# Performance work log

Measured on AMD Instinct MI355X. Metric: run time of the kernel, lower is better.

## Reference

```python
import jax, jax.numpy as jnp
import numpy as np

TOPK, NUM_CLASSES, ALPHA, BETA, EPS = 13, 80, 1.0, 6.0, 1e-9
IOU_EPS = 1e-7  # eps used inside bbox_iou (ultralytics default)


def ciou(box1, box2):
    # box1, box2: broadcastable [..., 4] in xyxy format; returns CIoU [..., 1]
    b1x1, b1y1, b1x2, b1y2 = jnp.split(box1, 4, axis=-1)
    b2x1, b2y1, b2x2, b2y2 = jnp.split(box2, 4, axis=-1)
    w1, h1 = b1x2 - b1x1, b1y2 - b1y1 + IOU_EPS
    w2, h2 = b2x2 - b2x1, b2y2 - b2y1 + IOU_EPS
    inter = (jnp.clip(jnp.minimum(b1x2, b2x2) - jnp.maximum(b1x1, b2x1), 0.0) *
             jnp.clip(jnp.minimum(b1y2, b2y2) - jnp.maximum(b1y1, b2y1), 0.0))
    union = w1 * h1 + w2 * h2 - inter + IOU_EPS
    iou = inter / union
    cw = jnp.maximum(b1x2, b2x2) - jnp.minimum(b1x1, b2x1)  # enclosing box width
    ch = jnp.maximum(b1y2, b2y2) - jnp.minimum(b1y1, b2y1)
    c2 = cw ** 2 + ch ** 2 + IOU_EPS
    rho2 = ((b2x1 + b2x2 - b1x1 - b1x2) ** 2 + (b2y1 + b2y2 - b1y1 - b1y2) ** 2) / 4.0
    v = (4.0 / np.pi ** 2) * (jnp.arctan(w2 / h2) - jnp.arctan(w1 / h1)) ** 2
    alpha = jax.lax.stop_gradient(v / (v - iou + (1.0 + IOU_EPS)))  # torch: with no_grad
    return iou - (rho2 / c2 + v * alpha)


def tal_forward(pd_scores, pd_bboxes, anc_points, gt_labels, gt_bboxes, mask_gt):
    bs, na, nc = pd_scores.shape
    nb = gt_bboxes.shape[1]
    dt = pd_scores.dtype
    mgt = mask_gt[..., 0]  # (b, nb)

    # --- select_candidates_in_gts: anchor center strictly inside gt box ---
    lt, rb = gt_bboxes[..., :2], gt_bboxes[..., 2:]
    deltas = jnp.concatenate([anc_points[None, None, :, :] - lt[:, :, None, :],
                              rb[:, :, None, :] - anc_points[None, None, :, :]], axis=-1)  # (b,nb,na,4)
    mask_in_gts = (deltas.min(-1) > EPS).astype(dt)  # (b,nb,na)
    valid = (mask_in_gts * mgt[:, :, None]) > 0  # bool (b,nb,na)

    # --- get_box_metrics: class score gather + pairwise CIoU, masked ---
    lbl = gt_labels[..., 0].astype(jnp.int32)  # (b,nb)
    scores = jnp.take_along_axis(pd_scores, lbl[:, None, :], axis=2)  # (b,na,nb)
    bbox_scores = jnp.where(valid, scores.transpose(0, 2, 1), 0.0)  # (b,nb,na)
    ov = ciou(gt_bboxes[:, :, None, :], pd_bboxes[:, None, :, :])[..., 0]  # (b,nb,na)
    overlaps = jnp.where(valid, jnp.clip(ov, 0.0), 0.0)
    align_metric = bbox_scores ** ALPHA * overlaps ** BETA

    # --- select_topk_candidates ---
    _, tk_i = jax.lax.top_k(align_metric, TOPK)  # (b,nb,TOPK)
    tk_i = jnp.where(mgt[:, :, None] > 0, tk_i, 0)  # invalid gt rows -> all idx 0 (counted >1 -> zeroed)
    flat_i = tk_i.reshape(bs * nb, TOPK)
    cnt = jnp.zeros((bs * nb, na), jnp.int32).at[jnp.arange(bs * nb)[:, None], flat_i].add(1)
    cnt = cnt.reshape(bs, nb, na)
    is_in_topk = jnp.where(cnt > 1, 0, cnt).astype(dt)
    mask_pos = is_in_topk * mask_in_gts * mgt[:, :, None]

    # --- select_highest_overlaps: resolve anchors claimed by multiple gts ---
    fg = mask_pos.sum(-2)  # (b,na)
    mask_multi = fg[:, None, :] > 1
    max_idx = overlaps.argmax(1)  # (b,na)
    is_max = jax.nn.one_hot(max_idx, nb, dtype=dt).transpose(0, 2, 1)  # (b,nb,na)
    mask_pos = jnp.where(mask_multi, is_max, mask_pos)
    fg_mask = mask_pos.sum(-2)  # (b,na)
    target_gt_idx = mask_pos.argmax(-2)  # (b,na)

    # --- get_targets ---
    flat_gt_idx = target_gt_idx + jnp.arange(bs)[:, None] * nb  # (b,na)
    target_labels = jnp.clip(lbl.reshape(-1)[flat_gt_idx], 0)
    target_bboxes = gt_bboxes.reshape(-1, 4)[flat_gt_idx]  # (b,na,4)
    target_scores = jax.nn.one_hot(target_labels, nc, dtype=dt)
    target_scores = jnp.where(fg_mask[..., None] > 0, target_scores, 0.0)

    # --- normalization of align metric ---
    align_metric = align_metric * mask_pos
    pos_align = align_metric.max(-1, keepdims=True)  # (b,nb,1)
    pos_over = (overlaps * mask_pos).max(-1, keepdims=True)
    norm = (align_metric * pos_over / (pos_align + EPS)).max(-2)[..., None]  # (b,na,1)
    target_scores = target_scores * norm
    return target_labels, target_bboxes, target_scores, fg_mask > 0, target_gt_idx


def _make_boxes(key, shape):
    kc, kw = jax.random.split(key)
    c = jax.random.uniform(kc, shape[:-1] + (2,), jnp.float32, 60.0, 580.0)
    wh = jax.random.uniform(kw, shape[:-1] + (2,), jnp.float32, 20.0, 120.0)
    return jnp.concatenate([c - wh / 2, c + wh / 2], axis=-1)


def setup_inputs() -> dict:
    key = jax.random.key(0)
    ks = jax.random.split(key, 6)
    bs, na, nc, nb = 32, 8400, 80, 64
    pd_scores = jax.random.uniform(ks[0], (bs, na, nc), jnp.float32)
    pd_bboxes = _make_boxes(ks[1], (bs, na, 4))
    anc_points = jax.random.uniform(ks[2], (na, 2), jnp.float32, 0.0, 640.0)
    gt_labels = jax.random.randint(ks[3], (bs, nb, 1), 0, nc, dtype=jnp.int32)
    gt_bboxes = _make_boxes(ks[4], (bs, nb, 4))
    mask_gt = (jax.random.uniform(ks[5], (bs, nb, 1)) < 0.8).astype(jnp.float32)
    return {"pd_scores": pd_scores, "pd_bboxes": pd_bboxes, "anc_points": anc_points,
            "gt_labels": gt_labels, "gt_bboxes": gt_bboxes, "mask_gt": mask_gt}


def reference(pd_scores, pd_bboxes, anc_points, gt_labels, gt_bboxes, mask_gt):
    return tal_forward(pd_scores, pd_bboxes, anc_points, gt_labels, gt_bboxes, mask_gt)
```

## Files before the change

### kernel.cpp

```cpp
#include <hip/hip_runtime.h>
#include <stdint.h>

#pragma clang fp contract(off)

#define BS 32
#define NB 64
#define NA 8400
#define NC 80
#define TK 13
#define QCAP 640
#define CMAX (QCAP + 32)
#define FORCED 32

typedef float floatx4 __attribute__((ext_vector_type(4)));

__device__ __forceinline__ float ciou_f(float g0, float g1, float g2, float g3,
                                        float p0, float p1, float p2, float p3) {
    const float E = 1e-7f;
    float w1 = g2 - g0, h1 = (g3 - g1) + E;
    float w2 = p2 - p0, h2 = (p3 - p1) + E;
    float iw = fminf(g2, p2) - fmaxf(g0, p0); iw = fmaxf(iw, 0.f);
    float ih = fminf(g3, p3) - fmaxf(g1, p1); ih = fmaxf(ih, 0.f);
    float inter = iw * ih;
    float uni = w1 * h1 + w2 * h2 - inter + E;
    float iou = inter / uni;
    float cw = fmaxf(g2, p2) - fminf(g0, p0);
    float ch = fmaxf(g3, p3) - fminf(g1, p1);
    float c2 = cw * cw + ch * ch + E;
    float dx = p0 + p2 - g0 - g2;
    float dy = p1 + p3 - g1 - g3;
    float rho2 = (dx * dx + dy * dy) / 4.0f;
    float da = atanf(w2 / h2) - atanf(w1 / h1);
    float v = 0.4052847345693511f * (da * da);
    float alpha = v / ((v - iou) + 1.0000001f);
    return iou - (rho2 / c2 + v * alpha);
}

__global__ __launch_bounds__(256) void k1a_scan(
    const float* __restrict__ anc,
    const float* __restrict__ gt_bboxes,
    const float* __restrict__ mask_gt,
    int* __restrict__ qcnt, int* __restrict__ qlist)
{
    int b = blockIdx.y;
    int a = blockIdx.x * 256 + threadIdx.x;
    if (a >= NA) return;
    float2 ap = *(const float2*)&anc[2 * a];
    for (int j = 0; j < NB; j++) {
        int r = b * NB + j;
        float mg = mask_gt[r];
        float gx = gt_bboxes[r * 4 + 0], gy = gt_bboxes[r * 4 + 1];
        float gz = gt_bboxes[r * 4 + 2], gw = gt_bboxes[r * 4 + 3];
        float d0 = ap.x - gx, d1 = ap.y - gy, d2 = gz - ap.x, d3 = gw - ap.y;
        float dmin = fminf(fminf(d0, d1), fminf(d2, d3));
        if (mg > 0.f && dmin > 1e-9f) {
            int p = atomicAdd(&qcnt[r], 1);
            if (p < QCAP) qlist[r * QCAP + p] = a;
        }
    }
}

__global__ __launch_bounds__(64) void k1b_topk(
    const float* __restrict__ pd_scores,
    const float* __restrict__ pd_bboxes,
    const float* __restrict__ anc,
    const int* __restrict__ gt_labels,
    const float* __restrict__ gt_bboxes,
    const float* __restrict__ mask_gt,
    const int* __restrict__ qcnt, const int* __restrict__ qlist,
    int* __restrict__ tk_a, float* __restrict__ tk_v,
    float* __restrict__ tk_o, int* __restrict__ tk_f)
{
    int r = blockIdx.x;
    int b = r >> 6;
    int lane = threadIdx.x;

    if (mask_gt[r] <= 0.f) {
        if (lane < TK) {
            tk_a[r * TK + lane] = 0; tk_v[r * TK + lane] = 0.f;
            tk_o[r * TK + lane] = 0.f; tk_f[r * TK + lane] = 0;
        }
        return;
    }

    __shared__ int   ca[CMAX];
    __shared__ float cv[CMAX];
    __shared__ float co[CMAX];

    float4 g = *(const float4*)&gt_bboxes[r * 4];
    int lbl = gt_labels[r];
    int n0 = min(qcnt[r], QCAP);

    bool add = false;
    if (lane < FORCED) {
        float2 ap = *(const float2*)&anc[2 * lane];
        float d0 = ap.x - g.x, d1 = ap.y - g.y, d2 = g.z - ap.x, d3 = g.w - ap.y;
        float dmin = fminf(fminf(d0, d1), fminf(d2, d3));
        add = !(dmin > 1e-9f);
    }
    unsigned long long mb = __ballot(add);
    int pos = __popcll(mb & ((1ull << lane) - 1ull));
    if (add) { ca[n0 + pos] = lane; cv[n0 + pos] = 0.f; co[n0 + pos] = 0.f; }
    int n = n0 + __popcll(mb);

    for (int c = lane; c < n0; c += 64) {
        int a = qlist[r * QCAP + c];
        float4 p = *(const float4*)&pd_bboxes[(b * NA + a) * 4];
        float ov = fmaxf(ciou_f(g.x, g.y, g.z, g.w, p.x, p.y, p.z, p.w), 0.f);
        float sc = pd_scores[(b * NA + a) * NC + lbl];
        float o2 = ov * ov;
        ca[c] = a | (1 << 30); cv[c] = sc * (o2 * o2 * o2); co[c] = ov;
    }
    __syncthreads();

    unsigned consumed = 0;
    int wslot = 0; float wval = 0.f;
    for (int round = 0; round < TK; round++) {
        float bv = -2.f; int bgi = 0x7fffffff; int bsl = 0;
        int li = 0;
        for (int c = lane; c < n; c += 64, li++) {
            if (consumed & (1u << li)) continue;
            float v = cv[c]; int gi = ca[c] & 0x3fffffff;
            if (v > bv || (v == bv && gi < bgi)) { bv = v; bgi = gi; bsl = c; }
        }
        for (int off = 32; off; off >>= 1) {
            float v2 = __shfl_down(bv, off);
            int  gi2 = __shfl_down(bgi, off);
            int  sl2 = __shfl_down(bsl, off);
            if (v2 > bv || (v2 == bv && gi2 < bgi)) { bv = v2; bgi = gi2; bsl = sl2; }
        }
        int wsl = __shfl(bsl, 0);
        float wv = __shfl(bv, 0);
        if ((wsl & 63) == lane) consumed |= 1u << (wsl >> 6);
        if (lane == round) { wslot = wsl; wval = wv; }
    }
    if (lane < TK) {
        int packed = ca[wslot]; int a = packed & 0x3fffffff; int in = (packed >> 30) & 1;
        tk_a[r * TK + lane] = a;
        tk_v[r * TK + lane] = wval;
        tk_o[r * TK + lane] = co[wslot];
        tk_f[r * TK + lane] = in;
    }
}

__global__ void k2a_init(int* cnt, int* jA, unsigned* posA, unsigned* posO,
                         int* mcount, int* qcnt) {
    int i = blockIdx.x * 256 + threadIdx.x;
    if (i < BS * NA) { cnt[i] = 0; jA[i] = -1; }
    if (i < BS * NB) { posA[i] = 0u; posO[i] = 0u; qcnt[i] = 0; }
    if (i == 0) *mcount = 0;
}

__global__ void k2b_count(const int* __restrict__ tk_a, const int* __restrict__ tk_f,
                          int* __restrict__ cnt) {
    int c = blockIdx.x * 256 + threadIdx.x;
    if (c >= BS * NB * TK) return;
    if (!tk_f[c]) return;
    int r = c / TK; int b = r >> 6;
    atomicAdd(&cnt[b * NA + tk_a[c]], 1);
}

__global__ void k2c_single(const int* __restrict__ tk_a, const float* __restrict__ tk_v,
                           const float* __restrict__ tk_o, const int* __restrict__ tk_f,
                           const int* __restrict__ cnt, int* __restrict__ jA,
                           float* __restrict__ av,
                           unsigned* __restrict__ posA, unsigned* __restrict__ posO,
                           int* __restrict__ mlist, int* __restrict__ mcount) {
    int c = blockIdx.x * 256 + threadIdx.x;
    if (c >= BS * NB * TK) return;
    if (!tk_f[c]) return;
    int r = c / TK; int b = r >> 6; int j = r & 63;
    int a = tk_a[c];
    int i = b * NA + a;
    if (cnt[i] == 1) {
        jA[i] = j; av[i] = tk_v[c];
        atomicMax(&posA[b * NB + j], __float_as_uint(tk_v[c]));
        atomicMax(&posO[b * NB + j], __float_as_uint(tk_o[c]));
    } else {
        int old = atomicCAS(&jA[i], -1, -2);
        if (old == -1) { int p = atomicAdd(mcount, 1); mlist[p] = i; }
    }
}

__global__ __launch_bounds__(256) void k2d_multi(
    const float* __restrict__ pd_scores,
    const float* __restrict__ pd_bboxes,
    const float* __restrict__ anc,
    const int* __restrict__ gt_labels,
    const float* __restrict__ gt_bboxes,
    const float* __restrict__ mask_gt,
    const int* __restrict__ mlist, const int* __restrict__ mcount,
    int* __restrict__ jA, float* __restrict__ av,
    unsigned* __restrict__ posA, unsigned* __restrict__ posO)
{
    int wid = (blockIdx.x * 256 + threadIdx.x) >> 6;
    int lane = threadIdx.x & 63;
    int nwaves = (gridDim.x * 256) >> 6;
    int nm = *mcount;
    for (int e = wid; e < nm; e += nwaves) {
        int i = mlist[e];
        int b = i / NA, a = i - b * NA;
        float2 ap = *(const float2*)&anc[2 * a];
        int row = b * NB + lane;
        float o = 0.f;
        if (mask_gt[row] > 0.f) {
            float4 g = *(const float4*)&gt_bboxes[row * 4];
            float d0 = ap.x - g.x, d1 = ap.y - g.y, d2 = g.z - ap.x, d3 = g.w - ap.y;
            float dmin = fminf(fminf(d0, d1), fminf(d2, d3));
            if (dmin > 1e-9f) {
                float4 p = *(const float4*)&pd_bboxes[(b * NA + a) * 4];
                o = fmaxf(ciou_f(g.x, g.y, g.z, g.w, p.x, p.y, p.z, p.w), 0.f);
            }
        }
        float bv = o; int bj = lane;
        for (int off = 32; off; off >>= 1) {
            float v2 = __shfl_down(bv, off);
            int  j2 = __shfl_down(bj, off);
            if (v2 > bv || (v2 == bv && j2 < bj)) { bv = v2; bj = j2; }
        }
        if (lane == 0) {
            int lbl = gt_labels[b * NB + bj];
            float sc = pd_scores[(b * NA + a) * NC + lbl];
            float o2 = bv * bv;
            float alg = sc * (o2 * o2 * o2);
            jA[i] = bj; av[i] = alg;
            atomicMax(&posA[b * NB + bj], __float_as_uint(alg));
            atomicMax(&posO[b * NB + bj], __float_as_uint(bv));
        }
    }
}

__global__ void k2f_final(const int* __restrict__ gt_labels,
                          const float* __restrict__ gt_bboxes,
                          const int* __restrict__ jA, const float* __restrict__ av,
                          const unsigned* __restrict__ posA, const unsigned* __restrict__ posO,
                          float* __restrict__ out,
                          float* __restrict__ normw, int* __restrict__ clsw) {
    int i = blockIdx.x * 256 + threadIdx.x;
    if (i >= BS * NA) return;
    int b = i / NA;
    int jj = jA[i];
    int tg = jj < 0 ? 0 : jj;
    int lab = gt_labels[b * NB + tg]; lab = lab < 0 ? 0 : lab;

    float* o_lab  = out;
    float* o_bbox = out + BS * NA;
    float* o_fg   = out + BS * NA * (5 + NC);
    float* o_idx  = o_fg + BS * NA;

    o_lab[i] = (float)lab;
    float4 bb = *(const float4*)&gt_bboxes[(b * NB + tg) * 4];
    *(float4*)&o_bbox[i * 4] = bb;
    o_fg[i] = (jj >= 0) ? 1.f : 0.f;
    o_idx[i] = (float)tg;

    float nrm = 0.f;
    if (jj >= 0) {
        float pa = __uint_as_float(posA[b * NB + jj]);
        float po = __uint_as_float(posO[b * NB + jj]);
        nrm = (av[i] * po) / (pa + 1e-9f);
    }
    normw[i] = nrm;
    clsw[i] = (jj >= 0) ? lab : -1;
}

__global__ void k3_scores(const float* __restrict__ normw, const int* __restrict__ clsw,
                          float* __restrict__ out) {
    int t = blockIdx.x * 256 + threadIdx.x;
    int row = t / 20;
    int c4 = (t - row * 20) * 4;
    int cls = clsw[row];
    float nv = normw[row];
    floatx4 v;
    v.x = (c4 + 0 == cls) ? nv : 0.f;
    v.y = (c4 + 1 == cls) ? nv : 0.f;
    v.z = (c4 + 2 == cls) ? nv : 0.f;
    v.w = (c4 + 3 == cls) ? nv : 0.f;
    float* o_sc = out + BS * NA * 5;
    __builtin_nontemporal_store(v, (floatx4*)&o_sc[row * NC + c4]);
}

extern "C" void kernel_launch(void* const* d_in, const int* in_sizes, int n_in,
                              void* d_out, int out_size, void* d_ws, size_t ws_size,
                              hipStream_t stream) {
    const float* pd_scores = (const float*)d_in[0];
    const float* pd_bboxes = (const float*)d_in[1];
    const float* anc       = (const float*)d_in[2];
    const int*   gt_labels = (const int*)d_in[3];
    const float* gt_bboxes = (const float*)d_in[4];
    const float* mask_gt   = (const float*)d_in[5];
    float* out = (float*)d_out;

    char* w = (char*)d_ws;
    const int NCAND = BS * NB * TK;
    int*      tk_a = (int*)w;      w += NCAND * 4;
    int*      tk_f = (int*)w;      w += NCAND * 4;
    float*    tk_v = (float*)w;    w += NCAND * 4;
    float*    tk_o = (float*)w;    w += NCAND * 4;
    int*      cnt  = (int*)w;      w += BS * NA * 4;
    int*      jA   = (int*)w;      w += BS * NA * 4;
    float*    av   = (float*)w;    w += BS * NA * 4;
    unsigned* posA = (unsigned*)w; w += BS * NB * 4;
    unsigned* posO = (unsigned*)w; w += BS * NB * 4;
    float*    normw = (float*)w;   w += BS * NA * 4;
    int*      clsw  = (int*)w;     w += BS * NA * 4;
    int*      mlist = (int*)w;     w += NCAND * 4;
    int*      mcount = (int*)w;    w += 64;
    int*      qcnt  = (int*)w;     w += BS * NB * 4;
    int*      qlist = (int*)w;     w += BS * NB * QCAP * 4;

    k2a_init<<<(BS * NA + 255) / 256, 256, 0, stream>>>(cnt, jA, posA, posO,
                                                        mcount, qcnt);
    {
        dim3 g((NA + 255) / 256, BS);
        k1a_scan<<<g, 256, 0, stream>>>(anc, gt_bboxes, mask_gt, qcnt, qlist);
    }
    k1b_topk<<<BS * NB, 64, 0, stream>>>(pd_scores, pd_bboxes, anc, gt_labels,
                                         gt_bboxes, mask_gt, qcnt, qlist,
                                         tk_a, tk_v, tk_o, tk_f);
    k2b_count<<<(NCAND + 255) / 256, 256, 0, stream>>>(tk_a, tk_f, cnt);
    k2c_single<<<(NCAND + 255) / 256, 256, 0, stream>>>(tk_a, tk_v, tk_o, tk_f,
                                                        cnt, jA, av, posA, posO,
                                                        mlist, mcount);
    k2d_multi<<<52, 256, 0, stream>>>(pd_scores, pd_bboxes, anc, gt_labels,
                                      gt_bboxes, mask_gt, mlist, mcount,
                                      jA, av, posA, posO);
    k2f_final<<<(BS * NA + 255) / 256, 256, 0, stream>>>(gt_labels, gt_bboxes, jA, av,
                                                         posA, posO, out, normw, clsw);
    k3_scores<<<(BS * NA * NC / 4 + 255) / 256, 256, 0, stream>>>(normw, clsw, out);
}
```

Baseline: 253.0 us.

## Aggregate scan atomics per wave, fuse count and final kernels, memset init

The candidate scan now uses a wave ballot so that one atomicAdd per wave reserves queue slots, instead of one atomic per hit. The per-anchor count atomics move into the top-k kernel, and the per-anchor finalisation is folded into the score-writing kernel, removing the normw/clsw intermediates. The init kernel becomes a single hipMemsetAsync over a contiguous zeroed region, with jA re-encoded so that 0 means unassigned. This removes three launches and extra global traffic, but the fused final kernel recomputes per-row values in each of 20 threads and the queue slot order may differ.

```diff
diff --git a/kernel.cpp b/kernel.cpp
--- a/kernel.cpp
+++ b/kernel.cpp
@@ -44,18 +44,25 @@
 {
     int b = blockIdx.y;
     int a = blockIdx.x * 256 + threadIdx.x;
-    if (a >= NA) return;
-    float2 ap = *(const float2*)&anc[2 * a];
+    int lane = threadIdx.x & 63;
+    bool inrange = a < NA;
+    float2 ap = inrange ? *(const float2*)&anc[2 * a] : make_float2(-1.f, -1.f);
     for (int j = 0; j < NB; j++) {
         int r = b * NB + j;
         float mg = mask_gt[r];
-        float gx = gt_bboxes[r * 4 + 0], gy = gt_bboxes[r * 4 + 1];
-        float gz = gt_bboxes[r * 4 + 2], gw = gt_bboxes[r * 4 + 3];
-        float d0 = ap.x - gx, d1 = ap.y - gy, d2 = gz - ap.x, d3 = gw - ap.y;
+        float4 g = *(const float4*)&gt_bboxes[r * 4];
+        float d0 = ap.x - g.x, d1 = ap.y - g.y, d2 = g.z - ap.x, d3 = g.w - ap.y;
         float dmin = fminf(fminf(d0, d1), fminf(d2, d3));
-        if (mg > 0.f && dmin > 1e-9f) {
-            int p = atomicAdd(&qcnt[r], 1);
-            if (p < QCAP) qlist[r * QCAP + p] = a;
+        bool hit = inrange && (mg > 0.f) && (dmin > 1e-9f);
+        unsigned long long m = __ballot(hit);
+        if (m) {
+            int rank = __popcll(m & ((1ull << lane) - 1ull));
+            int ldr = __ffsll((long long)m) - 1;
+            int base = 0;
+            if (lane == ldr) base = atomicAdd(&qcnt[r], __popcll(m));
+            base = __shfl(base, ldr);
+            int p = base + rank;
+            if (hit && p < QCAP) qlist[r * QCAP + p] = a;
         }
     }
 }
@@ -69,7 +76,8 @@
     const float* __restrict__ mask_gt,
     const int* __restrict__ qcnt, const int* __restrict__ qlist,
     int* __restrict__ tk_a, float* __restrict__ tk_v,
-    float* __restrict__ tk_o, int* __restrict__ tk_f)
+    float* __restrict__ tk_o, int* __restrict__ tk_f,
+    int* __restrict__ cnt)
 {
     int r = blockIdx.x;
     int b = r >> 6;
@@ -140,24 +148,8 @@
         tk_v[r * TK + lane] = wval;
         tk_o[r * TK + lane] = co[wslot];
         tk_f[r * TK + lane] = in;
-    }
-}
-
-__global__ void k2a_init(int* cnt, int* jA, unsigned* posA, unsigned* posO,
-                         int* mcount, int* qcnt) {
-    int i = blockIdx.x * 256 + threadIdx.x;
-    if (i < BS * NA) { cnt[i] = 0; jA[i] = -1; }
-    if (i < BS * NB) { posA[i] = 0u; posO[i] = 0u; qcnt[i] = 0; }
-    if (i == 0) *mcount = 0;
-}
-
-__global__ void k2b_count(const int* __restrict__ tk_a, const int* __restrict__ tk_f,
-                          int* __restrict__ cnt) {
-    int c = blockIdx.x * 256 + threadIdx.x;
-    if (c >= BS * NB * TK) return;
-    if (!tk_f[c]) return;
-    int r = c / TK; int b = r >> 6;
-    atomicAdd(&cnt[b * NA + tk_a[c]], 1);
+        if (in) atomicAdd(&cnt[b * NA + a], 1);
+    }
 }
 
 __global__ void k2c_single(const int* __restrict__ tk_a, const float* __restrict__ tk_v,
@@ -173,12 +165,12 @@
     int a = tk_a[c];
     int i = b * NA + a;
     if (cnt[i] == 1) {
-        jA[i] = j; av[i] = tk_v[c];
+        jA[i] = j + 1; av[i] = tk_v[c];
         atomicMax(&posA[b * NB + j], __float_as_uint(tk_v[c]));
         atomicMax(&posO[b * NB + j], __float_as_uint(tk_o[c]));
     } else {
-        int old = atomicCAS(&jA[i], -1, -2);
-        if (old == -1) { int p = atomicAdd(mcount, 1); mlist[p] = i; }
+        int old = atomicCAS(&jA[i], 0, -1);
+        if (old == 0) { int p = atomicAdd(mcount, 1); mlist[p] = i; }
     }
 }
 
@@ -223,61 +215,56 @@
             float sc = pd_scores[(b * NA + a) * NC + lbl];
             float o2 = bv * bv;
             float alg = sc * (o2 * o2 * o2);
-            jA[i] = bj; av[i] = alg;
+            jA[i] = bj + 1; av[i] = alg;
             atomicMax(&posA[b * NB + bj], __float_as_uint(alg));
             atomicMax(&posO[b * NB + bj], __float_as_uint(bv));
         }
     }
 }
 
-__global__ void k2f_final(const int* __restrict__ gt_labels,
-                          const float* __restrict__ gt_bboxes,
-                          const int* __restrict__ jA, const float* __restrict__ av,
-                          const unsigned* __restrict__ posA, const unsigned* __restrict__ posO,
-                          float* __restrict__ out,
-                          float* __restrict__ normw, int* __restrict__ clsw) {
-    int i = blockIdx.x * 256 + threadIdx.x;
-    if (i >= BS * NA) return;
-    int b = i / NA;
-    int jj = jA[i];
-    int tg = jj < 0 ? 0 : jj;
-    int lab = gt_labels[b * NB + tg]; lab = lab < 0 ? 0 : lab;
-
-    float* o_lab  = out;
-    float* o_bbox = out + BS * NA;
-    float* o_fg   = out + BS * NA * (5 + NC);
-    float* o_idx  = o_fg + BS * NA;
-
-    o_lab[i] = (float)lab;
-    float4 bb = *(const float4*)&gt_bboxes[(b * NB + tg) * 4];
-    *(float4*)&o_bbox[i * 4] = bb;
-    o_fg[i] = (jj >= 0) ? 1.f : 0.f;
-    o_idx[i] = (float)tg;
-
-    float nrm = 0.f;
-    if (jj >= 0) {
-        float pa = __uint_as_float(posA[b * NB + jj]);
-        float po = __uint_as_float(posO[b * NB + jj]);
-        nrm = (av[i] * po) / (pa + 1e-9f);
-    }
-    normw[i] = nrm;
-    clsw[i] = (jj >= 0) ? lab : -1;
-}
-
-__global__ void k3_scores(const float* __restrict__ normw, const int* __restrict__ clsw,
-                          float* __restrict__ out) {
+__global__ __launch_bounds__(256) void k3_final(
+    const int* __restrict__ gt_labels,
+    const float* __restrict__ gt_bboxes,
+    const int* __restrict__ jA, const float* __restrict__ av,
+    const unsigned* __restrict__ posA, const unsigned* __restrict__ posO,
+    float* __restrict__ out)
+{
     int t = blockIdx.x * 256 + threadIdx.x;
     int row = t / 20;
-    int c4 = (t - row * 20) * 4;
-    int cls = clsw[row];
-    float nv = normw[row];
+    int q = t - row * 20;
+    int b = row / NA;
+    int jj1 = jA[row];
+    int tg = jj1 > 0 ? jj1 - 1 : 0;
+    int lab = gt_labels[b * NB + tg]; lab = lab < 0 ? 0 : lab;
+
+    float nrm = 0.f;
+    if (jj1 > 0) {
+        float pa = __uint_as_float(posA[b * NB + tg]);
+        float po = __uint_as_float(posO[b * NB + tg]);
+        nrm = (av[row] * po) / (pa + 1e-9f);
+    }
+
+    int c4 = q * 4;
+    int cls = (jj1 > 0) ? lab : -1;
     floatx4 v;
-    v.x = (c4 + 0 == cls) ? nv : 0.f;
-    v.y = (c4 + 1 == cls) ? nv : 0.f;
-    v.z = (c4 + 2 == cls) ? nv : 0.f;
-    v.w = (c4 + 3 == cls) ? nv : 0.f;
+    v.x = (c4 + 0 == cls) ? nrm : 0.f;
+    v.y = (c4 + 1 == cls) ? nrm : 0.f;
+    v.z = (c4 + 2 == cls) ? nrm : 0.f;
+    v.w = (c4 + 3 == cls) ? nrm : 0.f;
     float* o_sc = out + BS * NA * 5;
     __builtin_nontemporal_store(v, (floatx4*)&o_sc[row * NC + c4]);
+
+    if (q == 0) {
+        float* o_lab  = out;
+        float* o_bbox = out + BS * NA;
+        float* o_fg   = out + BS * NA * (5 + NC);
+        float* o_idx  = o_fg + BS * NA;
+        o_lab[row] = (float)lab;
+        float4 bb = *(const float4*)&gt_bboxes[(b * NB + tg) * 4];
+        *(float4*)&o_bbox[row * 4] = bb;
+        o_fg[row] = (jj1 > 0) ? 1.f : 0.f;
+        o_idx[row] = (float)tg;
+    }
 }
 
 extern "C" void kernel_launch(void* const* d_in, const int* in_sizes, int n_in,
@@ -293,39 +280,36 @@
 
     char* w = (char*)d_ws;
     const int NCAND = BS * NB * TK;
+    char* zbase = w;
+    int*      cnt  = (int*)w;      w += BS * NA * 4;
+    int*      jA   = (int*)w;      w += BS * NA * 4;
+    int*      qcnt = (int*)w;      w += BS * NB * 4;
+    unsigned* posA = (unsigned*)w; w += BS * NB * 4;
+    unsigned* posO = (unsigned*)w; w += BS * NB * 4;
+    int*      mcount = (int*)w;    w += 64;
+    size_t zbytes = (size_t)(w - zbase);
+    float*    av   = (float*)w;    w += BS * NA * 4;
     int*      tk_a = (int*)w;      w += NCAND * 4;
     int*      tk_f = (int*)w;      w += NCAND * 4;
     float*    tk_v = (float*)w;    w += NCAND * 4;
     float*    tk_o = (float*)w;    w += NCAND * 4;
-    int*      cnt  = (int*)w;      w += BS * NA * 4;
-    int*      jA   = (int*)w;      w += BS * NA * 4;
-    float*    av   = (float*)w;    w += BS * NA * 4;
-    unsigned* posA = (unsigned*)w; w += BS * NB * 4;
-    unsigned* posO = (unsigned*)w; w += BS * NB * 4;
-    float*    normw = (float*)w;   w += BS * NA * 4;
-    int*      clsw  = (int*)w;     w += BS * NA * 4;
     int*      mlist = (int*)w;     w += NCAND * 4;
-    int*      mcount = (int*)w;    w += 64;
-    int*      qcnt  = (int*)w;     w += BS * NB * 4;
     int*      qlist = (int*)w;     w += BS * NB * QCAP * 4;
 
-    k2a_init<<<(BS * NA + 255) / 256, 256, 0, stream>>>(cnt, jA, posA, posO,
-                                                        mcount, qcnt);
+    hipMemsetAsync(zbase, 0, zbytes, stream);
     {
         dim3 g((NA + 255) / 256, BS);
         k1a_scan<<<g, 256, 0, stream>>>(anc, gt_bboxes, mask_gt, qcnt, qlist);
     }
     k1b_topk<<<BS * NB, 64, 0, stream>>>(pd_scores, pd_bboxes, anc, gt_labels,
                                          gt_bboxes, mask_gt, qcnt, qlist,
-                                         tk_a, tk_v, tk_o, tk_f);
-    k2b_count<<<(NCAND + 255) / 256, 256, 0, stream>>>(tk_a, tk_f, cnt);
+                                         tk_a, tk_v, tk_o, tk_f, cnt);
     k2c_single<<<(NCAND + 255) / 256, 256, 0, stream>>>(tk_a, tk_v, tk_o, tk_f,
                                                         cnt, jA, av, posA, posO,
                                                         mlist, mcount);
     k2d_multi<<<52, 256, 0, stream>>>(pd_scores, pd_bboxes, anc, gt_labels,
                                       gt_bboxes, mask_gt, mlist, mcount,
                                       jA, av, posA, posO);
-    k2f_final<<<(BS * NA + 255) / 256, 256, 0, stream>>>(gt_labels, gt_bboxes, jA, av,
-                                                         posA, posO, out, normw, clsw);
-    k3_scores<<<(BS * NA * NC / 4 + 255) / 256, 256, 0, stream>>>(normw, clsw, out);
-}
+    k3_final<<<BS * NA * 20 / 256, 256, 0, stream>>>(gt_labels, gt_bboxes, jA, av,
+                                                     posA, posO, out);
+}
```

Measured after the change: 263.1 us. +4.0%, slower.
